# Optimization experiments

Measured on AMD Instinct MI355X. Metric: run time of the kernel, lower is better.

The kernel has to match this reference:

```python
import jax, jax.numpy as jnp
import numpy as np

DIM, HEADS, FFN, E = 1024, 16, 4096, 8
B, S = 2, 1024
EPS = 1e-5


def _ln(x, g, b):
    mu = jnp.mean(x, axis=-1, keepdims=True)
    var = jnp.mean((x - mu) ** 2, axis=-1, keepdims=True)
    return (x - mu) * jax.lax.rsqrt(var + EPS) * g + b


def setup_inputs() -> dict:
    key = jax.random.key(0)
    ks = jax.random.split(key, 20)
    sd = 0.02
    d, f = DIM, FFN
    return {
        "x": jax.random.normal(ks[0], (B, S, d), jnp.float32),
        "ln1_g": jnp.ones((d,), jnp.float32), "ln1_b": jnp.zeros((d,), jnp.float32),
        "Wqkv": jax.random.normal(ks[1], (d, 3 * d), jnp.float32) * sd,
        "bqkv": jnp.zeros((3 * d,), jnp.float32),
        "Wo": jax.random.normal(ks[2], (d, d), jnp.float32) * sd,
        "bo": jnp.zeros((d,), jnp.float32),
        "ln2_g": jnp.ones((d,), jnp.float32), "ln2_b": jnp.zeros((d,), jnp.float32),
        "gate_w": jax.random.normal(ks[3], (d, E), jnp.float32) * sd,
        "W1": jax.random.normal(ks[4], (E, d, f), jnp.float32) * sd,
        "b1": jnp.zeros((E, f), jnp.float32),
        "W2": jax.random.normal(ks[5], (E, f, d), jnp.float32) * sd,
        "b2": jnp.zeros((E, d), jnp.float32),
        "rW1": jax.random.normal(ks[6], (d, f), jnp.float32) * sd,
        "rb1": jnp.zeros((f,), jnp.float32),
        "rW2": jax.random.normal(ks[7], (f, d), jnp.float32) * sd,
        "rb2": jnp.zeros((d,), jnp.float32),
        "coef_w": jax.random.normal(ks[8], (d, 2), jnp.float32) * sd,
        "coef_b": jnp.zeros((2,), jnp.float32),
    }


def reference(x, ln1_g, ln1_b, Wqkv, bqkv, Wo, bo, ln2_g, ln2_b, gate_w,
              W1, b1, W2, b2, rW1, rb1, rW2, rb2, coef_w, coef_b):
    b, s, d = x.shape
    h, dh = HEADS, d // HEADS

    # --- attention block ---
    xn = _ln(x, ln1_g, ln1_b)
    qkv = xn @ Wqkv + bqkv                       # [b,s,3d]
    q, k, v = jnp.split(qkv, 3, axis=-1)
    q = q.reshape(b, s, h, dh)
    k = k.reshape(b, s, h, dh)
    v = v.reshape(b, s, h, dh)
    scores = jnp.einsum("bqhd,bkhd->bhqk", q, k) / jnp.sqrt(jnp.float32(dh))
    attn = jax.nn.softmax(scores, axis=-1)
    ctx = jnp.einsum("bhqk,bkhd->bqhd", attn, v).reshape(b, s, d)
    x = x + ctx @ Wo + bo

    # --- MoE FFN block (top-1 gating, DeepSpeed residual MoE) ---
    xn2 = _ln(x, ln2_g, ln2_b)
    xt = xn2.reshape(b * s, d)                   # [T,d] tokens
    probs = jax.nn.softmax(xt @ gate_w, axis=-1)  # [T,E]
    gate_val = jnp.max(probs, axis=-1, keepdims=True)   # top-1 prob
    expert_idx = jnp.argmax(probs, axis=-1)
    oh = jax.nn.one_hot(expert_idx, E, dtype=xt.dtype)  # [T,E] dispatch mask

    xe = jnp.einsum("te,td->etd", oh, xt)        # dispatch [E,T,d]
    he = jax.nn.gelu(jnp.einsum("etd,edf->etf", xe, W1) + b1[:, None, :], approximate=False)
    ye = jnp.einsum("etf,efd->etd", he, W2) + b2[:, None, :]
    moe_out = jnp.einsum("te,etd->td", oh, ye) * gate_val  # combine [T,d]

    # residual dense expert + learned mixing coefficient
    rm = jax.nn.gelu(xt @ rW1 + rb1, approximate=False) @ rW2 + rb2
    coef = jax.nn.softmax(xt @ coef_w + coef_b, axis=-1)  # [T,2]
    ff = moe_out * coef[:, 0:1] + rm * coef[:, 1:2]

    return x + ff.reshape(b, s, d)
```

## Files before the change

kernel.cpp:

```cpp
#include <hip/hip_runtime.h>
#include <math.h>

#define TOK 2048
#define NDIM 1024

typedef __attribute__((ext_vector_type(4))) float f32x4;
typedef __attribute__((ext_vector_type(8))) short s16x8;
typedef __attribute__((ext_vector_type(4))) short s16x4;

__device__ __forceinline__ short f2bf(float x) {
  unsigned int u = __builtin_bit_cast(unsigned int, x);
  unsigned int r = (u + 0x7fffu + ((u >> 16) & 1u)) >> 16;
  return (short)r;
}
__device__ __forceinline__ void gload_lds16(const void* g, void* l) {
  __builtin_amdgcn_global_load_lds((const __attribute__((address_space(1))) void*)g,
                                   (__attribute__((address_space(3))) void*)l, 16, 0, 0);
}

struct PackP { const float* src; short* dst; int K, N, nkt; };

__device__ __forceinline__ void pack_body(const PackP& p, int bx, int by, int tid, char* smem)
{
  short (*T)[264] = (short(*)[264])smem;
  const int nkt = p.nkt;
  const int cb = bx / nkt, kt = bx % nkt;
  const int ntn = p.N >> 7;
  const float* src = p.src + (size_t)by * p.K * p.N + (size_t)(kt * 64) * p.N + cb * 256;
  #pragma unroll
  for (int i = 0; i < 16; ++i) {
    const int r = i * 4 + (tid >> 6);
    const f32x4 v = *(const f32x4*)(src + (size_t)r * p.N + (tid & 63) * 4);
    short* d = &T[r][(tid & 63) * 4];
    d[0] = f2bf(v[0]); d[1] = f2bf(v[1]); d[2] = f2bf(v[2]); d[3] = f2bf(v[3]);
  }
  __syncthreads();
  #pragma unroll
  for (int j = 0; j < 2; ++j) {
    short* dst = p.dst + ((size_t)(by * ntn + cb * 2 + j) * nkt + kt) * 8192;
    #pragma unroll
    for (int jj = 0; jj < 4; ++jj) {
      const int ch = tid * 4 + jj;
      const int col = ch >> 3, od = ch & 7, o = od ^ (col & 7);
      s16x8 v;
      #pragma unroll
      for (int kk = 0; kk < 8; ++kk) v[kk] = T[o * 8 + kk][j * 128 + col];
      *(s16x8*)(dst + ch * 8) = v;
    }
  }
}

__global__ __launch_bounds__(256)
void pack_k(PackP p)
{
  __shared__ char smem[34816];
  pack_body(p, blockIdx.x, blockIdx.y, threadIdx.x, smem);
}

__global__ __launch_bounds__(256)
void ln_k(const float* __restrict__ x, const float* __restrict__ g,
          const float* __restrict__ bb, short* __restrict__ out)
{
  const int row = blockIdx.x, tid = threadIdx.x;
  const f32x4 xv = *(const f32x4*)(x + (size_t)row * NDIM + tid * 4);
  float s = xv[0] + xv[1] + xv[2] + xv[3];
  float s2 = xv[0]*xv[0] + xv[1]*xv[1] + xv[2]*xv[2] + xv[3]*xv[3];
  #pragma unroll
  for (int m = 1; m < 64; m <<= 1) { s += __shfl_xor(s, m); s2 += __shfl_xor(s2, m); }
  __shared__ float red[8];
  const int w = tid >> 6, l = tid & 63;
  if (l == 0) { red[w] = s; red[4 + w] = s2; }
  __syncthreads();
  s = red[0] + red[1] + red[2] + red[3];
  s2 = red[4] + red[5] + red[6] + red[7];
  const float mean = s * (1.0f / NDIM);
  const float var = s2 * (1.0f / NDIM) - mean * mean;
  const float rstd = rsqrtf(var + 1e-5f);
  const f32x4 gv = *(const f32x4*)(g + tid * 4);
  const f32x4 bv = *(const f32x4*)(bb + tid * 4);
  s16x4 ov;
  #pragma unroll
  for (int j = 0; j < 4; ++j) ov[j] = f2bf((xv[j] - mean) * rstd * gv[j] + bv[j]);
  *(s16x4*)(out + (size_t)row * NDIM + tid * 4) = ov;
}

__global__ __launch_bounds__(256)
void gate_k(const float* __restrict__ x1, const float* __restrict__ g,
            const float* __restrict__ bb, const float* __restrict__ gw,
            const float* __restrict__ cw, const float* __restrict__ cb,
            int* __restrict__ counts, int* __restrict__ bucket,
            float* __restrict__ gs, float* __restrict__ c1o)
{
  const int tid = threadIdx.x, l = tid & 63, w = tid >> 6;
  const int t = blockIdx.x * 4 + w;
  f32x4 xv[4];
  #pragma unroll
  for (int it = 0; it < 4; ++it)
    xv[it] = *(const f32x4*)(x1 + (size_t)t * NDIM + it * 256 + l * 4);
  float s = 0.f, s2 = 0.f;
  #pragma unroll
  for (int it = 0; it < 4; ++it)
    #pragma unroll
    for (int j = 0; j < 4; ++j) { s += xv[it][j]; s2 += xv[it][j] * xv[it][j]; }
  #pragma unroll
  for (int m = 1; m < 64; m <<= 1) { s += __shfl_xor(s, m); s2 += __shfl_xor(s2, m); }
  const float mean = s * (1.0f / NDIM);
  const float rstd = rsqrtf(s2 * (1.0f / NDIM) - mean * mean + 1e-5f);
  float acc[10];
  #pragma unroll
  for (int j = 0; j < 10; ++j) acc[j] = 0.f;
  #pragma unroll
  for (int it = 0; it < 4; ++it) {
    #pragma unroll
    for (int j = 0; j < 4; ++j) {
      const int d0 = it * 256 + l * 4 + j;
      const float xn = (xv[it][j] - mean) * rstd * g[d0] + bb[d0];
      const f32x4 g0 = *(const f32x4*)(gw + (size_t)d0 * 8);
      const f32x4 g1 = *(const f32x4*)(gw + (size_t)d0 * 8 + 4);
      #pragma unroll
      for (int q = 0; q < 4; ++q) { acc[q] += xn * g0[q]; acc[4 + q] += xn * g1[q]; }
      acc[8] += xn * cw[d0 * 2]; acc[9] += xn * cw[d0 * 2 + 1];
    }
  }
  #pragma unroll
  for (int j = 0; j < 10; ++j)
    #pragma unroll
    for (int m = 1; m < 64; m <<= 1) acc[j] += __shfl_xor(acc[j], m);
  if (l == 0) {
    int best = 0; float mx = acc[0];
    #pragma unroll
    for (int e = 1; e < 8; ++e) if (acc[e] > mx) { mx = acc[e]; best = e; }
    float se = 0.f;
    #pragma unroll
    for (int e = 0; e < 8; ++e) se += __expf(acc[e] - mx);
    const float gate_val = 1.0f / se;
    const float l0 = acc[8] + cb[0], l1 = acc[9] + cb[1];
    const float cmx = fmaxf(l0, l1);
    const float e0 = __expf(l0 - cmx), e1 = __expf(l1 - cmx);
    const float inv = 1.0f / (e0 + e1);
    const int pos = atomicAdd(&counts[best], 1);
    bucket[best * TOK + pos] = t;
    gs[t] = gate_val * e0 * inv;
    c1o[t] = e1 * inv;
  }
}

struct GemmP {
  const short* A; const short* A2; const short* Bp; const short* Bp2;
  const float* bias; const float* bias2;
  short* outh; short* outh2; float* outf;
  const float* resid; const float* gs; const float* c1;
  const int* bucket; const int* counts;
  int N, K, ktc, nmt;
};

template<int MODE>
__device__ __forceinline__ void gemm_body(const GemmP& p, int bx, int ey, int z,
                                          int tid, char* smem)
{
  char* Al = smem;
  char* Bl = smem + 16384;
  const int l = tid & 63, w = tid >> 6;
  const int wr = w >> 1, wc = w & 1;
  const int ntn = p.N >> 7, nkt = p.K >> 6;
  const int nwg = p.nmt * ntn;
  const int logical = (bx & 7) * (nwg >> 3) + (bx >> 3);
  const int nt = logical / p.nmt;
  const int mt = logical % p.nmt;
  const bool first = (z == 0);
  const int K = p.K, N = p.N;

  int e = 0, cnt = TOK;
  const int* bucket = nullptr;
  if (MODE >= 2) {
    e = ey;
    if (e < 8) {
      cnt = p.counts[e];
      if (mt * 128 >= cnt) return;
      bucket = p.bucket + e * TOK;
    }
  }
  const short* Abase = (MODE == 3 && e == 8) ? p.A2 : p.A;
  const float* bias = (MODE >= 2) ? (e < 8 ? p.bias + (size_t)e * N : p.bias2) : p.bias;
  const short* btile = (MODE >= 2)
      ? (e < 8 ? p.Bp + ((size_t)(e * ntn + nt) * nkt) * 8192
               : p.Bp2 + ((size_t)nt * nkt) * 8192)
      : p.Bp + ((size_t)nt * nkt) * 8192;

  const short* aptr[4];
  #pragma unroll
  for (int i = 0; i < 4; ++i) {
    const int rl = (i * 256 + tid) >> 3;
    int row;
    if (bucket) {
      const int bidx = mt * 128 + rl;
      row = bucket[bidx < cnt ? bidx : mt * 128];
    } else row = mt * 128 + rl;
    aptr[i] = Abase + (size_t)row * K + ((tid & 7) ^ (rl & 7)) * 8;
  }

  const int kt0 = z * p.ktc, kt1 = kt0 + p.ktc;

  f32x4 acc[4][4] = {};
  for (int kt = kt0; kt < kt1; ++kt) {
    const short* bsrc = btile + kt * 8192;
    #pragma unroll
    for (int j = 0; j < 4; ++j)
      gload_lds16(bsrc + (j * 256 + tid) * 8, Bl + (j * 256 + (tid & 192)) * 16);
    #pragma unroll
    for (int i = 0; i < 4; ++i)
      gload_lds16(aptr[i] + kt * 64, Al + (i * 256 + (tid & 192)) * 16);
    __syncthreads();
    #pragma unroll
    for (int ks = 0; ks < 2; ++ks) {
      const int octd0 = ks * 4 + (l >> 4);
      s16x8 af[4], bfr[4];
      #pragma unroll
      for (int mf = 0; mf < 4; ++mf) {
        const int r = wr * 64 + mf * 16 + (l & 15);
        af[mf] = *(const s16x8*)(Al + r * 128 + (octd0 ^ (r & 7)) * 16);
      }
      #pragma unroll
      for (int nf = 0; nf < 4; ++nf) {
        const int c2 = wc * 64 + nf * 16 + (l & 15);
        bfr[nf] = *(const s16x8*)(Bl + c2 * 128 + (octd0 ^ (c2 & 7)) * 16);
      }
      #pragma unroll
      for (int mf = 0; mf < 4; ++mf)
        #pragma unroll
        for (int nf = 0; nf < 4; ++nf)
          acc[mf][nf] = __builtin_amdgcn_mfma_f32_16x16x32_bf16(af[mf], bfr[nf], acc[mf][nf], 0, 0, 0);
    }
    __syncthreads();
  }

  short* oh = (MODE == 2) ? (e < 8 ? p.outh : p.outh2) : p.outh;
  #pragma unroll
  for (int mf = 0; mf < 4; ++mf) {
    #pragma unroll
    for (int i = 0; i < 4; ++i) {
      const int rloc = wr * 64 + mf * 16 + (l >> 4) * 4 + i;
      int grow; bool valid = true;
      if (bucket) {
        const int bidx = mt * 128 + rloc;
        valid = bidx < cnt;
        grow = valid ? bucket[bidx] : 0;
      } else grow = mt * 128 + rloc;
      float srow = 1.f;
      if (MODE == 3) srow = (e < 8) ? (valid ? p.gs[grow] : 0.f) : p.c1[grow];
      #pragma unroll
      for (int nf = 0; nf < 4; ++nf) {
        const int col = nt * 128 + wc * 64 + nf * 16 + (l & 15);
        const size_t off = (size_t)grow * N + col;
        const float bc = first ? bias[col] : 0.f;
        if (MODE == 0) {
          oh[off] = f2bf(acc[mf][nf][i] + bc);
        } else if (MODE == 1) {
          atomicAdd(&p.outf[off], acc[mf][nf][i] + bc + (first ? p.resid[off] : 0.f));
        } else if (MODE == 2) {
          const float v = acc[mf][nf][i] + bc;
          const float gv = 0.5f * v * (1.0f + erff(v * 0.70710678f));
          if (valid) oh[off] = f2bf(gv);
        } else if (MODE == 3) {
          if (valid)
            atomicAdd(&p.outf[off], (acc[mf][nf][i] + bc) * srow +
                      ((e == 8 && first) ? p.resid[off] : 0.f));
        }
      }
    }
  }
}

template<int MODE>
__global__ __launch_bounds__(256, 4)
void gemm_k(GemmP p)
{
  __shared__ char smem[32768];
  gemm_body<MODE>(p, blockIdx.x, blockIdx.y, blockIdx.z, threadIdx.x, smem);
}

__device__ __forceinline__ void attn_body(const short* __restrict__ qkv,
                                          short* __restrict__ ctx,
                                          int qt, int bh, int tid, char* smem)
{
  char* Klds = smem;
  char* Vlds = smem + 8192;
  char* Plds = smem + 16384;
  const int l = tid & 63, w = tid >> 6;
  const int b = bh >> 4, h = bh & 15;
  const size_t tbase = (size_t)b * 1024;

  const int sq = qt * 64 + w * 16 + (l & 15);
  s16x8 qf[2];
  #pragma unroll
  for (int ks = 0; ks < 2; ++ks)
    qf[ks] = *(const s16x8*)(qkv + (tbase + sq) * 3072 + h * 64 + ks * 32 + (l >> 4) * 8);

  f32x4 o[4] = {};
  float mrow[4], lrow[4];
  #pragma unroll
  for (int i = 0; i < 4; ++i) { mrow[i] = -1e30f; lrow[i] = 0.f; }

  for (int kt = 0; kt < 16; ++kt) {
    #pragma unroll
    for (int i = 0; i < 2; ++i) {
      const int s = i * 256 + tid;
      const int r = s >> 3, c = s & 7, csrc = c ^ (r & 7);
      const short* gsrc = qkv + (tbase + kt * 64 + r) * 3072 + 1024 + h * 64 + csrc * 8;
      gload_lds16(gsrc, Klds + (i * 256 + (tid & 192)) * 16);
    }
    #pragma unroll
    for (int i = 0; i < 2; ++i) {
      const int kv0 = (i * 4 + w) * 8;
      s16x8 vv;
      #pragma unroll
      for (int j = 0; j < 8; ++j)
        vv[j] = qkv[(tbase + kt * 64 + kv0 + j) * 3072 + 2048 + h * 64 + l];
      *(s16x8*)(Vlds + ((l * 128 + kv0 * 2) ^ ((l & 7) << 4))) = vv;
    }
    __syncthreads();

    f32x4 sv[4];
    #pragma unroll
    for (int nf = 0; nf < 4; ++nf) {
      f32x4 a = {0.f, 0.f, 0.f, 0.f};
      const int kv = nf * 16 + (l & 15);
      #pragma unroll
      for (int ks = 0; ks < 2; ++ks) {
        const s16x8 kb = *(const s16x8*)(Klds +
            ((kv * 128 + (ks * 32 + (l >> 4) * 8) * 2) ^ ((kv & 7) << 4)));
        a = __builtin_amdgcn_mfma_f32_16x16x32_bf16(qf[ks], kb, a, 0, 0, 0);
      }
      sv[nf] = a * 0.125f;
    }
    float sc[4], ps[4];
    #pragma unroll
    for (int i = 0; i < 4; ++i) {
      float m = fmaxf(fmaxf(sv[0][i], sv[1][i]), fmaxf(sv[2][i], sv[3][i]));
      #pragma unroll
      for (int msk = 1; msk < 16; msk <<= 1) m = fmaxf(m, __shfl_xor(m, msk));
      const float mn = fmaxf(mrow[i], m);
      sc[i] = __expf(mrow[i] - mn);
      mrow[i] = mn;
      ps[i] = 0.f;
    }
    #pragma unroll
    for (int nf = 0; nf < 4; ++nf)
      #pragma unroll
      for (int i = 0; i < 4; ++i) {
        const float pp = __expf(sv[nf][i] - mrow[i]);
        sv[nf][i] = pp;
        ps[i] += pp;
      }
    #pragma unroll
    for (int i = 0; i < 4; ++i) {
      #pragma unroll
      for (int msk = 1; msk < 16; msk <<= 1) ps[i] += __shfl_xor(ps[i], msk);
      lrow[i] = lrow[i] * sc[i] + ps[i];
    }
    #pragma unroll
    for (int nf = 0; nf < 4; ++nf)
      #pragma unroll
      for (int i = 0; i < 4; ++i) o[nf][i] *= sc[i];

    char* pw = Plds + w * 2048;
    #pragma unroll
    for (int nf = 0; nf < 4; ++nf)
      #pragma unroll
      for (int i = 0; i < 4; ++i) {
        const int q = (l >> 4) * 4 + i;
        *(short*)(pw + ((q * 128 + (nf * 16 + (l & 15)) * 2) ^ ((q & 7) << 4))) = f2bf(sv[nf][i]);
      }
    __syncthreads();
    #pragma unroll
    for (int ks = 0; ks < 2; ++ks) {
      const s16x8 pa = *(const s16x8*)(pw +
          (((l & 15) * 128 + (ks * 32 + (l >> 4) * 8) * 2) ^ ((l & 7) << 4)));
      #pragma unroll
      for (int nf = 0; nf < 4; ++nf) {
        const int dh = nf * 16 + (l & 15);
        const s16x8 vb = *(const s16x8*)(Vlds +
            ((dh * 128 + (ks * 32 + (l >> 4) * 8) * 2) ^ ((dh & 7) << 4)));
        o[nf] = __builtin_amdgcn_mfma_f32_16x16x32_bf16(pa, vb, o[nf], 0, 0, 0);
      }
    }
    __syncthreads();
  }
  #pragma unroll
  for (int i = 0; i < 4; ++i) {
    const float inv = 1.0f / lrow[i];
    const size_t t = tbase + qt * 64 + w * 16 + (l >> 4) * 4 + i;
    #pragma unroll
    for (int nf = 0; nf < 4; ++nf)
      ctx[t * 1024 + h * 64 + nf * 16 + (l & 15)] = f2bf(o[nf][i] * inv);
  }
}

__global__ __launch_bounds__(256, 4)
void qkvpack_k(GemmP g, PackP pWo, PackP pW1, PackP prW1)
{
  __shared__ char smem[34816];
  const int v = blockIdx.x;
  if (v < 384) {
    gemm_body<0>(g, v, 0, 0, threadIdx.x, smem);
  } else if (v < 448) {
    pack_body(pWo, v - 384, 0, threadIdx.x, smem);
  } else if (v < 2496) {
    const int u = v - 448;
    pack_body(pW1, u & 255, u >> 8, threadIdx.x, smem);
  } else {
    pack_body(prW1, v - 2496, 0, threadIdx.x, smem);
  }
}

__global__ __launch_bounds__(256, 2)
void attnpack_k(const short* qkv, short* ctx, PackP pW2, PackP prW2)
{
  __shared__ char smem[34816];
  const int v = blockIdx.x;
  if (v < 512) {
    attn_body(qkv, ctx, v & 15, v >> 4, threadIdx.x, smem);
  } else if (v < 2560) {
    const int u = v - 512;
    pack_body(pW2, u & 255, u >> 8, threadIdx.x, smem);
  } else {
    pack_body(prW2, v - 2560, 0, threadIdx.x, smem);
  }
}

extern "C" void kernel_launch(void* const* d_in, const int* in_sizes, int n_in,
                              void* d_out, int out_size, void* d_ws, size_t ws_size,
                              hipStream_t stream)
{
  const float* x    = (const float*)d_in[0];
  const float* ln1g = (const float*)d_in[1];
  const float* ln1b = (const float*)d_in[2];
  const float* Wqkv = (const float*)d_in[3];
  const float* bqkv = (const float*)d_in[4];
  const float* Wo   = (const float*)d_in[5];
  const float* bo   = (const float*)d_in[6];
  const float* ln2g = (const float*)d_in[7];
  const float* ln2b = (const float*)d_in[8];
  const float* gw   = (const float*)d_in[9];
  const float* W1   = (const float*)d_in[10];
  const float* b1   = (const float*)d_in[11];
  const float* W2   = (const float*)d_in[12];
  const float* b2   = (const float*)d_in[13];
  const float* rW1  = (const float*)d_in[14];
  const float* rb1  = (const float*)d_in[15];
  const float* rW2  = (const float*)d_in[16];
  const float* rb2  = (const float*)d_in[17];
  const float* cw   = (const float*)d_in[18];
  const float* cb   = (const float*)d_in[19];
  float* out = (float*)d_out;

  char* ws = (char*)d_ws;
  const size_t MB = 1024 * 1024;
  short* xn1    = (short*)(ws + 0);
  short* qkv    = (short*)(ws + 4 * MB);
  short* he     = (short*)(ws + 4 * MB);
  short* ctx    = (short*)(ws + 16 * MB);
  float* x1     = (float*)(ws + 20 * MB);
  short* xn2    = (short*)(ws + 28 * MB);
  short* hr     = (short*)(ws + 32 * MB);
  int*   counts = (int*)(ws + 56 * MB);
  int*   bucket = (int*)(ws + 56 * MB + 256);
  float* gs     = (float*)(ws + 56 * MB + 256 + 64 * 1024);
  float* c1     = (float*)(ws + 56 * MB + 256 + 64 * 1024 + 8192);
  short* Wqkvp  = (short*)(ws + 64 * MB);
  short* Wop    = (short*)(ws + 70 * MB);
  short* W1p    = (short*)(ws + 72 * MB);
  short* W2p    = (short*)(ws + 136 * MB);
  short* rW1p   = (short*)(ws + 200 * MB);
  short* rW2p   = (short*)(ws + 208 * MB);

  hipMemsetAsync(counts, 0, 8 * sizeof(int), stream);
  hipMemsetAsync(x1, 0, TOK * NDIM * sizeof(float), stream);
  hipMemsetAsync(out, 0, TOK * NDIM * sizeof(float), stream);

  PackP pk{Wqkv, Wqkvp, 1024, 3072, 16};
  pack_k<<<dim3(12 * 16, 1), 256, 0, stream>>>(pk);

  ln_k<<<TOK, 256, 0, stream>>>(x, ln1g, ln1b, xn1);

  GemmP p{};
  p.A = xn1; p.Bp = Wqkvp; p.bias = bqkv; p.outh = qkv;
  p.N = 3072; p.K = 1024; p.ktc = 16; p.nmt = 16;
  PackP pWo{Wo, Wop, 1024, 1024, 16};
  PackP pW1{W1, W1p, 1024, 4096, 16};
  PackP prW1{rW1, rW1p, 1024, 4096, 16};
  qkvpack_k<<<dim3(2752), 256, 0, stream>>>(p, pWo, pW1, prW1);

  PackP pW2{W2, W2p, 4096, 1024, 64};
  PackP prW2{rW2, rW2p, 4096, 1024, 64};
  attnpack_k<<<dim3(2816), 256, 0, stream>>>(qkv, ctx, pW2, prW2);

  p = GemmP{};
  p.A = ctx; p.Bp = Wop; p.bias = bo; p.outf = x1; p.resid = x;
  p.N = 1024; p.K = 1024; p.ktc = 8; p.nmt = 16;
  gemm_k<1><<<dim3(128, 1, 2), 256, 0, stream>>>(p);

  ln_k<<<TOK, 256, 0, stream>>>(x1, ln2g, ln2b, xn2);
  gate_k<<<TOK / 4, 256, 0, stream>>>(x1, ln2g, ln2b, gw, cw, cb, counts, bucket, gs, c1);

  p = GemmP{};
  p.A = xn2; p.Bp = W1p; p.Bp2 = rW1p; p.bias = b1; p.bias2 = rb1;
  p.outh = he; p.outh2 = hr; p.N = 4096; p.K = 1024; p.ktc = 16; p.nmt = 16;
  p.bucket = bucket; p.counts = counts;
  gemm_k<2><<<dim3(512, 9), 256, 0, stream>>>(p);

  p = GemmP{};
  p.A = he; p.A2 = hr; p.Bp = W2p; p.Bp2 = rW2p; p.bias = b2; p.bias2 = rb2;
  p.outf = out; p.resid = x1; p.gs = gs; p.c1 = c1;
  p.N = 1024; p.K = 4096; p.ktc = 32; p.nmt = 16;
  p.bucket = bucket; p.counts = counts;
  gemm_k<3><<<dim3(128, 9, 2), 256, 0, stream>>>(p);
}
```

Baseline: 435.6 us.

## Use 256x256 double-buffered GEMM tiles for MoE expert and residual FFN layers

```diff
diff --git a/kernel.cpp b/kernel.cpp
--- a/kernel.cpp
+++ b/kernel.cpp
@@ -20,12 +20,12 @@
 
 struct PackP { const float* src; short* dst; int K, N, nkt; };
 
+template<int WIDE>
 __device__ __forceinline__ void pack_body(const PackP& p, int bx, int by, int tid, char* smem)
 {
   short (*T)[264] = (short(*)[264])smem;
   const int nkt = p.nkt;
   const int cb = bx / nkt, kt = bx % nkt;
-  const int ntn = p.N >> 7;
   const float* src = p.src + (size_t)by * p.K * p.N + (size_t)(kt * 64) * p.N + cb * 256;
   #pragma unroll
   for (int i = 0; i < 16; ++i) {
@@ -35,17 +35,32 @@
     d[0] = f2bf(v[0]); d[1] = f2bf(v[1]); d[2] = f2bf(v[2]); d[3] = f2bf(v[3]);
   }
   __syncthreads();
-  #pragma unroll
-  for (int j = 0; j < 2; ++j) {
-    short* dst = p.dst + ((size_t)(by * ntn + cb * 2 + j) * nkt + kt) * 8192;
-    #pragma unroll
-    for (int jj = 0; jj < 4; ++jj) {
-      const int ch = tid * 4 + jj;
+  if (WIDE) {
+    const int ntn = p.N >> 8;
+    short* dst = p.dst + ((size_t)(by * ntn + cb) * nkt + kt) * 16384;
+    #pragma unroll
+    for (int jj = 0; jj < 8; ++jj) {
+      const int ch = tid * 8 + jj;
       const int col = ch >> 3, od = ch & 7, o = od ^ (col & 7);
       s16x8 v;
       #pragma unroll
-      for (int kk = 0; kk < 8; ++kk) v[kk] = T[o * 8 + kk][j * 128 + col];
+      for (int kk = 0; kk < 8; ++kk) v[kk] = T[o * 8 + kk][col];
       *(s16x8*)(dst + ch * 8) = v;
+    }
+  } else {
+    const int ntn = p.N >> 7;
+    #pragma unroll
+    for (int j = 0; j < 2; ++j) {
+      short* dst = p.dst + ((size_t)(by * ntn + cb * 2 + j) * nkt + kt) * 8192;
+      #pragma unroll
+      for (int jj = 0; jj < 4; ++jj) {
+        const int ch = tid * 4 + jj;
+        const int col = ch >> 3, od = ch & 7, o = od ^ (col & 7);
+        s16x8 v;
+        #pragma unroll
+        for (int kk = 0; kk < 8; ++kk) v[kk] = T[o * 8 + kk][j * 128 + col];
+        *(s16x8*)(dst + ch * 8) = v;
+      }
     }
   }
 }
@@ -54,7 +69,7 @@
 void pack_k(PackP p)
 {
   __shared__ char smem[34816];
-  pack_body(p, blockIdx.x, blockIdx.y, threadIdx.x, smem);
+  pack_body<0>(p, blockIdx.x, blockIdx.y, threadIdx.x, smem);
 }
 
 __global__ __launch_bounds__(256)
@@ -155,8 +170,7 @@
 };
 
 template<int MODE>
-__device__ __forceinline__ void gemm_body(const GemmP& p, int bx, int ey, int z,
-                                          int tid, char* smem)
+__device__ __forceinline__ void gemm_body(const GemmP& p, int bx, int z, int tid, char* smem)
 {
   char* Al = smem;
   char* Bl = smem + 16384;
@@ -169,38 +183,16 @@
   const int mt = logical % p.nmt;
   const bool first = (z == 0);
   const int K = p.K, N = p.N;
-
-  int e = 0, cnt = TOK;
-  const int* bucket = nullptr;
-  if (MODE >= 2) {
-    e = ey;
-    if (e < 8) {
-      cnt = p.counts[e];
-      if (mt * 128 >= cnt) return;
-      bucket = p.bucket + e * TOK;
-    }
-  }
-  const short* Abase = (MODE == 3 && e == 8) ? p.A2 : p.A;
-  const float* bias = (MODE >= 2) ? (e < 8 ? p.bias + (size_t)e * N : p.bias2) : p.bias;
-  const short* btile = (MODE >= 2)
-      ? (e < 8 ? p.Bp + ((size_t)(e * ntn + nt) * nkt) * 8192
-               : p.Bp2 + ((size_t)nt * nkt) * 8192)
-      : p.Bp + ((size_t)nt * nkt) * 8192;
+  const short* btile = p.Bp + ((size_t)nt * nkt) * 8192;
 
   const short* aptr[4];
   #pragma unroll
   for (int i = 0; i < 4; ++i) {
     const int rl = (i * 256 + tid) >> 3;
-    int row;
-    if (bucket) {
-      const int bidx = mt * 128 + rl;
-      row = bucket[bidx < cnt ? bidx : mt * 128];
-    } else row = mt * 128 + rl;
-    aptr[i] = Abase + (size_t)row * K + ((tid & 7) ^ (rl & 7)) * 8;
+    aptr[i] = p.A + (size_t)(mt * 128 + rl) * K + ((tid & 7) ^ (rl & 7)) * 8;
   }
 
   const int kt0 = z * p.ktc, kt1 = kt0 + p.ktc;
-
   f32x4 acc[4][4] = {};
   for (int kt = kt0; kt < kt1; ++kt) {
     const short* bsrc = btile + kt * 8192;
@@ -234,38 +226,18 @@
     __syncthreads();
   }
 
-  short* oh = (MODE == 2) ? (e < 8 ? p.outh : p.outh2) : p.outh;
   #pragma unroll
   for (int mf = 0; mf < 4; ++mf) {
     #pragma unroll
     for (int i = 0; i < 4; ++i) {
-      const int rloc = wr * 64 + mf * 16 + (l >> 4) * 4 + i;
-      int grow; bool valid = true;
-      if (bucket) {
-        const int bidx = mt * 128 + rloc;
-        valid = bidx < cnt;
-        grow = valid ? bucket[bidx] : 0;
-      } else grow = mt * 128 + rloc;
-      float srow = 1.f;
-      if (MODE == 3) srow = (e < 8) ? (valid ? p.gs[grow] : 0.f) : p.c1[grow];
+      const int grow = mt * 128 + wr * 64 + mf * 16 + (l >> 4) * 4 + i;
       #pragma unroll
       for (int nf = 0; nf < 4; ++nf) {
         const int col = nt * 128 + wc * 64 + nf * 16 + (l & 15);
         const size_t off = (size_t)grow * N + col;
-        const float bc = first ? bias[col] : 0.f;
-        if (MODE == 0) {
-          oh[off] = f2bf(acc[mf][nf][i] + bc);
-        } else if (MODE == 1) {
-          atomicAdd(&p.outf[off], acc[mf][nf][i] + bc + (first ? p.resid[off] : 0.f));
-        } else if (MODE == 2) {
-          const float v = acc[mf][nf][i] + bc;
-          const float gv = 0.5f * v * (1.0f + erff(v * 0.70710678f));
-          if (valid) oh[off] = f2bf(gv);
-        } else if (MODE == 3) {
-          if (valid)
-            atomicAdd(&p.outf[off], (acc[mf][nf][i] + bc) * srow +
-                      ((e == 8 && first) ? p.resid[off] : 0.f));
-        }
+        const float bc = first ? p.bias[col] : 0.f;
+        if (MODE == 0) p.outh[off] = f2bf(acc[mf][nf][i] + bc);
+        else atomicAdd(&p.outf[off], acc[mf][nf][i] + bc + (first ? p.resid[off] : 0.f));
       }
     }
   }
@@ -276,7 +248,139 @@
 void gemm_k(GemmP p)
 {
   __shared__ char smem[32768];
-  gemm_body<MODE>(p, blockIdx.x, blockIdx.y, blockIdx.z, threadIdx.x, smem);
+  gemm_body<MODE>(p, blockIdx.x, blockIdx.z, threadIdx.x, smem);
+}
+
+template<int MODE>
+__global__ __launch_bounds__(512, 1)
+void g256_k(GemmP p)
+{
+  __shared__ char Al[2][32768];
+  __shared__ char Bl[2][32768];
+  const int tid = threadIdx.x;
+  const int l = tid & 63, wid = tid >> 6;
+  const int wr = wid >> 2, wc = wid & 3;
+  const int ntn = p.N >> 8, nkt = p.K >> 6;
+  const int nwg = p.nmt * ntn;
+  const int logical = (blockIdx.x & 7) * (nwg >> 3) + (blockIdx.x >> 3);
+  const int nt = logical / p.nmt;
+  const int mt = logical % p.nmt;
+  const int z = blockIdx.z;
+  const bool first = (z == 0);
+  const int K = p.K, N = p.N;
+
+  const int e = blockIdx.y;
+  int cnt = TOK;
+  const int* bucket = nullptr;
+  if (e < 8) {
+    cnt = p.counts[e];
+    if (mt * 256 >= cnt) return;
+    bucket = p.bucket + e * TOK;
+  }
+  const short* Abase = (MODE == 3 && e == 8) ? p.A2 : p.A;
+  const float* bias = (e < 8) ? p.bias + (size_t)e * N : p.bias2;
+  const short* btile = (e < 8) ? p.Bp + ((size_t)(e * ntn + nt) * nkt) * 16384
+                               : p.Bp2 + ((size_t)nt * nkt) * 16384;
+
+  const short* aptr[4];
+  #pragma unroll
+  for (int j = 0; j < 4; ++j) {
+    const int rl = (j * 512 + tid) >> 3;
+    int row;
+    if (bucket) {
+      const int bidx = mt * 256 + rl;
+      row = bucket[bidx < cnt ? bidx : mt * 256];
+    } else row = mt * 256 + rl;
+    aptr[j] = Abase + (size_t)row * K + ((tid & 7) ^ (rl & 7)) * 8;
+  }
+
+  auto stage = [&](int kt, int b) {
+    const short* bsrc = btile + (size_t)kt * 16384;
+    #pragma unroll
+    for (int j = 0; j < 4; ++j)
+      gload_lds16(bsrc + (j * 512 + tid) * 8, Bl[b] + (j * 512 + (tid & 448)) * 16);
+    #pragma unroll
+    for (int j = 0; j < 4; ++j)
+      gload_lds16(aptr[j] + kt * 64, Al[b] + (j * 512 + (tid & 448)) * 16);
+  };
+
+  const int kt0 = z * p.ktc, kt1 = kt0 + p.ktc;
+  stage(kt0, 0);
+  if (kt0 + 1 < kt1) stage(kt0 + 1, 1);
+
+  f32x4 acc[4][4][2] = {};
+  for (int kt = kt0; kt < kt1; ++kt) {
+    const int cur = (kt - kt0) & 1;
+    if (kt + 1 < kt1) asm volatile("s_waitcnt vmcnt(8)" ::: "memory");
+    else              asm volatile("s_waitcnt vmcnt(0)" ::: "memory");
+    __builtin_amdgcn_s_barrier();
+    #pragma unroll
+    for (int q = 0; q < 4; ++q) {
+      s16x8 af[2][4], bfr[2][2];
+      #pragma unroll
+      for (int ks = 0; ks < 2; ++ks) {
+        const int octd0 = ks * 4 + (l >> 4);
+        #pragma unroll
+        for (int mf = 0; mf < 4; ++mf) {
+          const int r = wr * 128 + (q >> 1) * 64 + mf * 16 + (l & 15);
+          af[ks][mf] = *(const s16x8*)(Al[cur] + r * 128 + (octd0 ^ (r & 7)) * 16);
+        }
+        #pragma unroll
+        for (int nf = 0; nf < 2; ++nf) {
+          const int c2 = wc * 64 + (q & 1) * 32 + nf * 16 + (l & 15);
+          bfr[ks][nf] = *(const s16x8*)(Bl[cur] + c2 * 128 + (octd0 ^ (c2 & 7)) * 16);
+        }
+      }
+      __builtin_amdgcn_s_barrier();
+      __builtin_amdgcn_s_setprio(1);
+      #pragma unroll
+      for (int ks = 0; ks < 2; ++ks)
+        #pragma unroll
+        for (int mf = 0; mf < 4; ++mf)
+          #pragma unroll
+          for (int nf = 0; nf < 2; ++nf)
+            acc[q][mf][nf] = __builtin_amdgcn_mfma_f32_16x16x32_bf16(
+                af[ks][mf], bfr[ks][nf], acc[q][mf][nf], 0, 0, 0);
+      __builtin_amdgcn_s_setprio(0);
+      __builtin_amdgcn_s_barrier();
+    }
+    if (kt + 2 < kt1) stage(kt + 2, cur);
+  }
+
+  short* oh = (e < 8) ? p.outh : p.outh2;
+  #pragma unroll
+  for (int q = 0; q < 4; ++q) {
+    #pragma unroll
+    for (int mf = 0; mf < 4; ++mf) {
+      #pragma unroll
+      for (int i = 0; i < 4; ++i) {
+        const int rloc = wr * 128 + (q >> 1) * 64 + mf * 16 + (l >> 4) * 4 + i;
+        int grow; bool valid = true;
+        if (bucket) {
+          const int bidx = mt * 256 + rloc;
+          valid = bidx < cnt;
+          grow = valid ? bucket[bidx] : 0;
+        } else grow = mt * 256 + rloc;
+        float srow = 1.f;
+        if (MODE == 3) srow = (e < 8) ? (valid ? p.gs[grow] : 0.f) : p.c1[grow];
+        #pragma unroll
+        for (int nf = 0; nf < 2; ++nf) {
+          const int col = nt * 256 + wc * 64 + (q & 1) * 32 + nf * 16 + (l & 15);
+          const size_t off = (size_t)grow * N + col;
+          const float bc = first ? bias[col] : 0.f;
+          if (MODE == 2) {
+            const float v = acc[q][mf][nf][i] + bc;
+            const float gv = 0.5f * v * (1.0f + erff(v * 0.70710678f));
+            if (valid) oh[off] = f2bf(gv);
+          } else {
+            if (valid)
+              atomicAdd(&p.outf[off], (acc[q][mf][nf][i] + bc) * srow +
+                        ((e == 8 && first) ? p.resid[off] : 0.f));
+          }
+        }
+      }
+    }
+  }
 }
 
 __device__ __forceinline__ void attn_body(const short* __restrict__ qkv,
@@ -402,14 +506,14 @@
   __shared__ char smem[34816];
   const int v = blockIdx.x;
   if (v < 384) {
-    gemm_body<0>(g, v, 0, 0, threadIdx.x, smem);
+    gemm_body<0>(g, v, 0, threadIdx.x, smem);
   } else if (v < 448) {
-    pack_body(pWo, v - 384, 0, threadIdx.x, smem);
+    pack_body<0>(pWo, v - 384, 0, threadIdx.x, smem);
   } else if (v < 2496) {
     const int u = v - 448;
-    pack_body(pW1, u & 255, u >> 8, threadIdx.x, smem);
+    pack_body<1>(pW1, u & 255, u >> 8, threadIdx.x, smem);
   } else {
-    pack_body(prW1, v - 2496, 0, threadIdx.x, smem);
+    pack_body<1>(prW1, v - 2496, 0, threadIdx.x, smem);
   }
 }
 
@@ -422,9 +526,9 @@
     attn_body(qkv, ctx, v & 15, v >> 4, threadIdx.x, smem);
   } else if (v < 2560) {
     const int u = v - 512;
-    pack_body(pW2, u & 255, u >> 8, threadIdx.x, smem);
+    pack_body<1>(pW2, u & 255, u >> 8, threadIdx.x, smem);
   } else {
-    pack_body(prW2, v - 2560, 0, threadIdx.x, smem);
+    pack_body<1>(prW2, v - 2560, 0, threadIdx.x, smem);
   }
 }
 
@@ -505,14 +609,14 @@
 
   p = GemmP{};
   p.A = xn2; p.Bp = W1p; p.Bp2 = rW1p; p.bias = b1; p.bias2 = rb1;
-  p.outh = he; p.outh2 = hr; p.N = 4096; p.K = 1024; p.ktc = 16; p.nmt = 16;
+  p.outh = he; p.outh2 = hr; p.N = 4096; p.K = 1024; p.ktc = 16; p.nmt = 8;
   p.bucket = bucket; p.counts = counts;
-  gemm_k<2><<<dim3(512, 9), 256, 0, stream>>>(p);
+  g256_k<2><<<dim3(128, 9), 512, 0, stream>>>(p);
 
   p = GemmP{};
   p.A = he; p.A2 = hr; p.Bp = W2p; p.Bp2 = rW2p; p.bias = b2; p.bias2 = rb2;
   p.outf = out; p.resid = x1; p.gs = gs; p.c1 = c1;
-  p.N = 1024; p.K = 4096; p.ktc = 32; p.nmt = 16;
+  p.N = 1024; p.K = 4096; p.ktc = 16; p.nmt = 8;
   p.bucket = bucket; p.counts = counts;
-  gemm_k<3><<<dim3(128, 9, 2), 256, 0, stream>>>(p);
-}
+  g256_k<3><<<dim3(32, 9, 4), 512, 0, stream>>>(p);
+}
```

Result: slower. 1.062 ms (+143.8%).
